# Performance work log

Hardware: AMD Instinct MI355X
Metric: run time of the kernel (lower is better)

## Reference

```python
import jax, jax.numpy as jnp
import numpy as np

M, B, D, N = 8, 200000, 32, 100000
TINY = np.finfo(np.float32).tiny


def _vol(box):
    # box: (..., 2, D) with box[...,0,:]=z (min corner), box[...,1,:]=Z (max corner)
    side = jnp.clip(box[..., 1, :] - box[..., 0, :], 0.0, None)
    return jnp.prod(side, axis=-1)


def _intersection(a, b):
    z = jnp.maximum(a[..., 0, :], b[..., 0, :])
    Z = jnp.minimum(a[..., 1, :], b[..., 1, :])
    return jnp.stack((z, Z), axis=-2)


def setup_inputs() -> dict:
    key = jax.random.key(0)
    k1, k2, k3, k4 = jax.random.split(key, 4)
    z = jax.random.uniform(k1, (M, B, 1, D), dtype=jnp.float32) * 0.1
    Z = 0.9 + jax.random.uniform(k2, (M, B, 1, D), dtype=jnp.float32) * 0.1
    box_param = jnp.concatenate([z, Z], axis=2)  # (M, B, 2, D)
    weights = jax.random.normal(k3, (M,), dtype=jnp.float32)
    ids = jax.random.randint(k4, (N, 4), 0, B, dtype=jnp.int64)
    return {"box_param": box_param, "weights": weights, "ids": ids}


def reference(box_param, weights, ids):
    boxes = jnp.clip(box_param, 0.0, 1.0)  # default universe -> clamp to [0,1]
    w = jax.nn.softmax(weights)            # (M,)
    # default universe box has volume prod(1-0) = 1
    uz = jnp.zeros((D,), boxes.dtype)
    uZ = jnp.ones((D,), boxes.dtype)
    universe_vol = _vol(jnp.stack((uz, uZ), axis=-2))  # scalar 1.0

    def wsum(vols):  # vols: (M, N) -> (N,)
        return jnp.einsum('m,mn->n', w, vols)

    i0, i1, i2 = ids[:, 0], ids[:, 1], ids[:, 2]
    A = boxes[:, i0]   # (M, N, 2, D)
    Bb = boxes[:, i1]
    C = boxes[:, i2]

    unary_probs = wsum(_vol(A) / universe_vol)

    AiB = _intersection(A, Bb)
    two_vol = wsum(_vol(AiB) / universe_vol) + TINY
    two_div = wsum(_vol(A) / universe_vol) + TINY
    two_cond = jnp.exp(jnp.log(two_vol) - jnp.log(two_div))

    three_vol = wsum(_vol(_intersection(AiB, C)) / universe_vol) + TINY
    three_div = wsum(_vol(AiB) / universe_vol) + TINY
    three_cond = jnp.exp(jnp.log(three_vol) - jnp.log(three_div))

    unary_mask = i0 == i1
    three_mask = i1 != i2
    two_mask = jnp.logical_and(~three_mask, ~unary_mask)
    # torch writes unary, then two, then three -> three takes precedence
    probs = jnp.where(three_mask, three_cond,
            jnp.where(two_mask, two_cond,
            jnp.where(unary_mask, unary_probs, 0.0)))
    return probs
```

## Files before the change

kernel.cpp:

```cpp
#include <hip/hip_runtime.h>
#include <hip/hip_bf16.h>


#define MM 8
#define BB 200000
#define DD 32

__global__ __launch_bounds__(256) void box_triples_kernel(
    const float* __restrict__ box,
    const float* __restrict__ wts,
    const int*   __restrict__ ids,
    float*       __restrict__ out,
    int N)
{
    const int lane = threadIdx.x & 63;
    const int wave = threadIdx.x >> 6;
    const int n = blockIdx.x * (blockDim.x >> 6) + wave;
    if (n >= N) return;

    const int m = lane >> 3;
    const int t = lane & 7;

    const int4 idv = ((const int4*)ids)[n];
    const int i0 = idv.x, i1 = idv.y, i2 = idv.z;

    const int baseA = (m * BB + i0) * (2 * DD) + t * 4;
    const int baseB = (m * BB + i1) * (2 * DD) + t * 4;
    const int baseC = (m * BB + i2) * (2 * DD) + t * 4;

    const float4 zA4 = *(const float4*)(box + baseA);
    const float4 ZA4 = *(const float4*)(box + baseA + DD);
    const float4 zB4 = *(const float4*)(box + baseB);
    const float4 ZB4 = *(const float4*)(box + baseB + DD);
    const float4 zC4 = *(const float4*)(box + baseC);
    const float4 ZC4 = *(const float4*)(box + baseC + DD);

    float wl = wts[m];
    float wmax = wl;
    #pragma unroll
    for (int off = 8; off < 64; off <<= 1) wmax = fmaxf(wmax, __shfl_xor(wmax, off));
    float ew = __expf(wl - wmax);
    float esum = ew;
    #pragma unroll
    for (int off = 8; off < 64; off <<= 1) esum += __shfl_xor(esum, off);
    const float w = ew / esum;

    float pA = 1.f, pAB = 1.f, pABC = 1.f;
    #define CL(x) fminf(fmaxf((x), 0.f), 1.f)
    #define COMP(c) { \
        const float za = CL(zA4.c), Za = CL(ZA4.c); \
        const float zb = CL(zB4.c), Zb = CL(ZB4.c); \
        const float zc = CL(zC4.c), Zc = CL(ZC4.c); \
        const float zab  = fmaxf(za, zb),  Zab  = fminf(Za, Zb); \
        const float zabc = fmaxf(zab, zc), Zabc = fminf(Zab, Zc); \
        pA   *= fmaxf(Za   - za,   0.f); \
        pAB  *= fmaxf(Zab  - zab,  0.f); \
        pABC *= fmaxf(Zabc - zabc, 0.f); \
    }
    COMP(x) COMP(y) COMP(z) COMP(w)
    #undef COMP
    #undef CL

    #pragma unroll
    for (int off = 1; off < 8; off <<= 1) {
        pA   *= __shfl_xor(pA,   off);
        pAB  *= __shfl_xor(pAB,  off);
        pABC *= __shfl_xor(pABC, off);
    }

    float sA = w * pA, sAB = w * pAB, sABC = w * pABC;
    #pragma unroll
    for (int off = 8; off < 64; off <<= 1) {
        sA   += __shfl_xor(sA,   off);
        sAB  += __shfl_xor(sAB,  off);
        sABC += __shfl_xor(sABC, off);
    }

    const float TINY = 1.1754943508222875e-38f;
    float res;
    if (i1 != i2) {
        res = (sABC + TINY) / (sAB + TINY);
    } else if (i0 != i1) {
        res = (sAB + TINY) / (sA + TINY);
    } else {
        res = sA;
    }

    if (lane == 0) out[n] = res;
}

extern "C" void kernel_launch(void* const* d_in, const int* in_sizes, int n_in,
                              void* d_out, int out_size, void* d_ws, size_t ws_size,
                              hipStream_t stream) {
    const float* box = (const float*)d_in[0];
    const float* wts = (const float*)d_in[1];
    const int*   ids = (const int*)d_in[2];
    float* out = (float*)d_out;
    const int N = out_size;

    const int wavesPerBlock = 4;
    const int blocks = (N + wavesPerBlock - 1) / wavesPerBlock;
    box_triples_kernel<<<blocks, 256, 0, stream>>>(box, wts, ids, out, N);
}
```

Before: 528.4 us.

## Pre-transpose and clip boxes to index-major layout before gathering

Adds a pass that rewrites the box tensor from (M,B,2,D) to (B,M,2,D) with clamping applied, writing it to workspace. The gather kernel then reads each referenced box index as one contiguous 2KB block covering all mixture components, and skips the per-element clamps. This trades an extra full read and write of the box tensor on every call for more contiguous gather accesses. The original kernel remains as a fallback when the workspace is too small.

Measured after the change: 651.9 us. 23.4% more time.

```diff
diff --git a/kernel.cpp b/kernel.cpp
--- a/kernel.cpp
+++ b/kernel.cpp
@@ -6,7 +6,97 @@
 #define BB 200000
 #define DD 32
 
-__global__ __launch_bounds__(256) void box_triples_kernel(
+__global__ __launch_bounds__(256) void transpose_clip_kernel(
+    const float4* __restrict__ in, float4* __restrict__ out)
+{
+    const int idx = blockIdx.x * 256 + threadIdx.x;
+    const int t = idx & 7;
+    const int s = (idx >> 3) & 1;
+    const int m = (idx >> 4) & 7;
+    const int b = idx >> 7;
+    float4 v = in[((m * BB + b) * 2 + s) * 8 + t];
+    v.x = fminf(fmaxf(v.x, 0.f), 1.f);
+    v.y = fminf(fmaxf(v.y, 0.f), 1.f);
+    v.z = fminf(fmaxf(v.z, 0.f), 1.f);
+    v.w = fminf(fmaxf(v.w, 0.f), 1.f);
+    out[idx] = v;
+}
+
+__global__ __launch_bounds__(256) void gather_kernel(
+    const float* __restrict__ tbox,
+    const float* __restrict__ wts,
+    const int*   __restrict__ ids,
+    float*       __restrict__ out,
+    int N)
+{
+    const int lane = threadIdx.x & 63;
+    const int wave = threadIdx.x >> 6;
+    const int n = blockIdx.x * (blockDim.x >> 6) + wave;
+    if (n >= N) return;
+
+    const int m = lane >> 3;
+    const int t = lane & 7;
+
+    const int4 idv = ((const int4*)ids)[n];
+    const int i0 = idv.x, i1 = idv.y, i2 = idv.z;
+
+    const int baseA = i0 * (MM * 2 * DD) + m * (2 * DD) + t * 4;
+    const int baseB = i1 * (MM * 2 * DD) + m * (2 * DD) + t * 4;
+    const int baseC = i2 * (MM * 2 * DD) + m * (2 * DD) + t * 4;
+
+    const float4 zA4 = *(const float4*)(tbox + baseA);
+    const float4 ZA4 = *(const float4*)(tbox + baseA + DD);
+    const float4 zB4 = *(const float4*)(tbox + baseB);
+    const float4 ZB4 = *(const float4*)(tbox + baseB + DD);
+    const float4 zC4 = *(const float4*)(tbox + baseC);
+    const float4 ZC4 = *(const float4*)(tbox + baseC + DD);
+
+    float wl = wts[m];
+    float wmax = wl;
+    #pragma unroll
+    for (int off = 8; off < 64; off <<= 1) wmax = fmaxf(wmax, __shfl_xor(wmax, off));
+    float ew = __expf(wl - wmax);
+    float esum = ew;
+    #pragma unroll
+    for (int off = 8; off < 64; off <<= 1) esum += __shfl_xor(esum, off);
+    const float w = ew / esum;
+
+    float pA = 1.f, pAB = 1.f, pABC = 1.f;
+    #define COMP(c) { \
+        const float zab  = fmaxf(zA4.c, zB4.c),  Zab  = fminf(ZA4.c, ZB4.c); \
+        const float zabc = fmaxf(zab, zC4.c),    Zabc = fminf(Zab, ZC4.c); \
+        pA   *= fmaxf(ZA4.c - zA4.c, 0.f); \
+        pAB  *= fmaxf(Zab   - zab,   0.f); \
+        pABC *= fmaxf(Zabc  - zabc,  0.f); \
+    }
+    COMP(x) COMP(y) COMP(z) COMP(w)
+    #undef COMP
+
+    #pragma unroll
+    for (int off = 1; off < 8; off <<= 1) {
+        pA   *= __shfl_xor(pA,   off);
+        pAB  *= __shfl_xor(pAB,  off);
+        pABC *= __shfl_xor(pABC, off);
+    }
+
+    float sA = w * pA, sAB = w * pAB, sABC = w * pABC;
+    #pragma unroll
+    for (int off = 8; off < 64; off <<= 1) {
+        sA   += __shfl_xor(sA,   off);
+        sAB  += __shfl_xor(sAB,  off);
+        sABC += __shfl_xor(sABC, off);
+    }
+
+    const float TINY = 1.1754943508222875e-38f;
+    float res;
+    if (i1 != i2)      res = (sABC + TINY) / (sAB + TINY);
+    else if (i0 != i1) res = (sAB  + TINY) / (sA  + TINY);
+    else               res = sA;
+
+    if (lane == 0) out[n] = res;
+}
+
+__global__ __launch_bounds__(256) void direct_kernel(
     const float* __restrict__ box,
     const float* __restrict__ wts,
     const int*   __restrict__ ids,
@@ -78,13 +168,9 @@
 
     const float TINY = 1.1754943508222875e-38f;
     float res;
-    if (i1 != i2) {
-        res = (sABC + TINY) / (sAB + TINY);
-    } else if (i0 != i1) {
-        res = (sAB + TINY) / (sA + TINY);
-    } else {
-        res = sA;
-    }
+    if (i1 != i2)      res = (sABC + TINY) / (sAB + TINY);
+    else if (i0 != i1) res = (sAB  + TINY) / (sA  + TINY);
+    else               res = sA;
 
     if (lane == 0) out[n] = res;
 }
@@ -98,7 +184,16 @@
     float* out = (float*)d_out;
     const int N = out_size;
 
+    const size_t tbox_bytes = (size_t)BB * MM * 2 * DD * sizeof(float);
     const int wavesPerBlock = 4;
     const int blocks = (N + wavesPerBlock - 1) / wavesPerBlock;
-    box_triples_kernel<<<blocks, 256, 0, stream>>>(box, wts, ids, out, N);
+
+    if (ws_size >= tbox_bytes) {
+        float* tbox = (float*)d_ws;
+        transpose_clip_kernel<<<100000, 256, 0, stream>>>(
+            (const float4*)box, (float4*)tbox);
+        gather_kernel<<<blocks, 256, 0, stream>>>(tbox, wts, ids, out, N);
+    } else {
+        direct_kernel<<<blocks, 256, 0, stream>>>(box, wts, ids, out, N);
+    }
 }
```
